# Performance work log

Measured on AMD Instinct MI355X. Metric: run time of the kernel, lower is better.

The kernel has to match this reference:

```python
import jax, jax.numpy as jnp
import numpy as np

N = 50000
K = 4
D_IN = 256
D_OUT = 64
E = 800000

def setup_inputs() -> dict:
    key = jax.random.key(0)
    k1, k2, k3, k4, k5 = jax.random.split(key, 5)
    x = jax.random.normal(k1, (N, K, D_IN), dtype=jnp.float32)
    weight = jax.random.normal(k2, (D_IN, D_OUT), dtype=jnp.float32) * (1.0 / np.sqrt(D_IN))
    adj_rows = jax.random.randint(k3, (E,), 0, N, dtype=jnp.int32)
    adj_cols = jax.random.randint(k4, (E,), 0, N, dtype=jnp.int32)
    adj_vals = jax.random.uniform(k5, (E,), dtype=jnp.float32)
    return {"x": x, "weight": weight, "adj_rows": adj_rows, "adj_cols": adj_cols, "adj_vals": adj_vals}

def reference(x, weight, adj_rows, adj_cols, adj_vals):
    # x: [N, K, D_in]; weight: [D_in, D_out]
    # dropout p=0.0 / eval mode -> identity
    # support = x @ W for every sample k, vectorized over K
    support = jnp.einsum('nkd,df->nkf', x, weight)          # [N, K, D_out]
    # sparse adj matmul: out[r] += vals[e] * support[cols[e]]
    msgs = adj_vals[:, None, None] * support[adj_cols]       # [E, K, D_out]
    out = jax.ops.segment_sum(msgs, adj_rows, num_segments=N)  # [N, K, D_out]
    return jax.nn.relu(out)
```

## Files before the change

kernel.cpp:

```cpp
#include <hip/hip_runtime.h>
#include <stdint.h>

#define D_IN   256
#define D_OUT  64
#define KHEADS 4
#define ROWLEN 256
#define GBM    128
#define LDW    264
#define CAP    128

typedef __attribute__((ext_vector_type(8))) short bf16x8;
typedef __attribute__((ext_vector_type(4))) float f32x4;

__device__ __forceinline__ unsigned cvt_pk_bf16(float lo, float hi) {
  unsigned r;
  asm("v_cvt_pk_bf16_f32 %0, %1, %2" : "=v"(r) : "v"(lo), "v"(hi));
  return r;
}

__device__ __forceinline__ bf16x8 pack8(float4 a, float4 b) {
  union { unsigned u[4]; bf16x8 v; } r;
  r.u[0] = cvt_pk_bf16(a.x, a.y);
  r.u[1] = cvt_pk_bf16(a.z, a.w);
  r.u[2] = cvt_pk_bf16(b.x, b.y);
  r.u[3] = cvt_pk_bf16(b.z, b.w);
  return r.v;
}

__device__ __forceinline__ void gemm_body(const float* __restrict__ X,
                                          const float* __restrict__ W,
                                          signed char* __restrict__ Sq,
                                          float* __restrict__ scaleArr,
                                          int M, int Nnodes, int gb) {
  __shared__ unsigned short lWt[64 * LDW];
  const int t    = threadIdx.x;
  const int wave = t >> 6;
  const int lane = t & 63;
  const int q    = lane >> 4;
  const int l16  = lane & 15;
  const long row0 = (long)gb * GBM;

#pragma unroll
  for (int j = 0; j < 16; ++j) {
    int flat = t + j * 256;
    int kr   = flat >> 4;
    int nn   = (flat & 15) << 2;
    float4 v = *(const float4*)&W[(size_t)kr * D_OUT + nn];
    unsigned p0 = cvt_pk_bf16(v.x, v.y);
    unsigned p1 = cvt_pk_bf16(v.z, v.w);
    lWt[(nn + 0) * LDW + kr] = (unsigned short)(p0 & 0xffffu);
    lWt[(nn + 1) * LDW + kr] = (unsigned short)(p0 >> 16);
    lWt[(nn + 2) * LDW + kr] = (unsigned short)(p1 & 0xffffu);
    lWt[(nn + 3) * LDW + kr] = (unsigned short)(p1 >> 16);
  }
  __syncthreads();

  long r0 = row0 + wave * 32 + l16;       if (r0 > (long)M - 1) r0 = M - 1;
  long r1 = row0 + wave * 32 + 16 + l16;  if (r1 > (long)M - 1) r1 = M - 1;
  const float* __restrict__ x0 = X + r0 * D_IN + q * 8;
  const float* __restrict__ x1 = X + r1 * D_IN + q * 8;

  f32x4 acc[2][4];
#pragma unroll
  for (int rb = 0; rb < 2; ++rb)
#pragma unroll
    for (int cb = 0; cb < 4; ++cb) acc[rb][cb] = (f32x4){0.f, 0.f, 0.f, 0.f};

  float4 c00 = *(const float4*)(x0);
  float4 c01 = *(const float4*)(x0 + 4);
  float4 c10 = *(const float4*)(x1);
  float4 c11 = *(const float4*)(x1 + 4);
#pragma unroll
  for (int s = 0; s < 8; ++s) {
    float4 n00, n01, n10, n11;
    if (s < 7) {
      const float* p0 = x0 + (s + 1) * 32;
      const float* p1 = x1 + (s + 1) * 32;
      n00 = *(const float4*)(p0); n01 = *(const float4*)(p0 + 4);
      n10 = *(const float4*)(p1); n11 = *(const float4*)(p1 + 4);
    }
    bf16x8 a0 = pack8(c00, c01);
    bf16x8 a1 = pack8(c10, c11);
    const unsigned short* wb = &lWt[l16 * LDW + s * 32 + q * 8];
#pragma unroll
    for (int cb = 0; cb < 4; ++cb) {
      bf16x8 b = *(const bf16x8*)(wb + cb * 16 * LDW);
      acc[0][cb] = __builtin_amdgcn_mfma_f32_16x16x32_bf16(a0, b, acc[0][cb], 0, 0, 0);
      acc[1][cb] = __builtin_amdgcn_mfma_f32_16x16x32_bf16(a1, b, acc[1][cb], 0, 0, 0);
    }
    if (s < 7) { c00 = n00; c01 = n01; c10 = n10; c11 = n11; }
  }

  float nm0 = 0.f, nm1 = 0.f;
#pragma unroll
  for (int cb = 0; cb < 4; ++cb)
#pragma unroll
    for (int reg = 0; reg < 4; ++reg) {
      nm0 = fmaxf(nm0, fabsf(acc[0][cb][reg]));
      nm1 = fmaxf(nm1, fabsf(acc[1][cb][reg]));
    }
#pragma unroll
  for (int d = 1; d < 16; d <<= 1) {
    nm0 = fmaxf(nm0, __shfl_xor(nm0, d, 64));
    nm1 = fmaxf(nm1, __shfl_xor(nm1, d, 64));
  }
  const float inv0 = (nm0 > 0.f) ? 127.f / nm0 : 0.f;
  const float inv1 = (nm1 > 0.f) ? 127.f / nm1 : 0.f;
  const int node_base = gb * 32 + wave * 8;
  if (l16 == 0) {
    int n0 = node_base + q;
    int n1 = node_base + 4 + q;
    if (n0 < Nnodes) scaleArr[n0] = nm0 / 127.f;
    if (n1 < Nnodes) scaleArr[n1] = nm1 / 127.f;
  }
#pragma unroll
  for (int rb = 0; rb < 2; ++rb) {
    const float inv = rb ? inv1 : inv0;
#pragma unroll
    for (int cb = 0; cb < 4; ++cb)
#pragma unroll
      for (int reg = 0; reg < 4; ++reg) {
        long r = row0 + wave * 32 + rb * 16 + q * 4 + reg;
        if (r < M) {
          int qi = (int)rintf(acc[rb][cb][reg] * inv);
          Sq[r * D_OUT + cb * 16 + l16] = (signed char)qi;
        }
      }
  }
}

__device__ __forceinline__ void place_body(const int* __restrict__ rows,
                                           const int* __restrict__ cols,
                                           const float* __restrict__ vals,
                                           int* __restrict__ cnt,
                                           uint2* __restrict__ ecv, int E, int pb) {
  int e = pb * 256 + threadIdx.x;
  if (e < E) {
    int r = rows[e];
    int c = cols[e];
    float v = vals[e];
    int pos = atomicAdd(&cnt[r], 1);
    if (pos < CAP)
      ecv[((size_t)r << 7) + pos] = make_uint2((unsigned)c, __float_as_uint(v));
  }
}

__global__ __launch_bounds__(256) void fused_phase1(
    const float* __restrict__ X, const float* __restrict__ W,
    signed char* __restrict__ Sq, float* __restrict__ scaleArr,
    const int* __restrict__ rows, const int* __restrict__ cols,
    const float* __restrict__ vals, int* __restrict__ cnt,
    uint2* __restrict__ ecv, int M, int Nnodes, int E, int G, int P) {
  const int bid = blockIdx.x;
  const int g = bid / 3, r3 = bid - 3 * g;
  if (r3 == 0) {
    if (g < G) gemm_body(X, W, Sq, scaleArr, M, Nnodes, g);
  } else {
    int pb = 2 * g + r3 - 1;
    if (pb < P) place_body(rows, cols, vals, cnt, ecv, E, pb);
  }
}

__global__ __launch_bounds__(256) void gather_kernel(const int* __restrict__ Sqi,
                                                     const float* __restrict__ scaleArr,
                                                     const int* __restrict__ cnt,
                                                     const uint2* __restrict__ ecv,
                                                     float* __restrict__ out, int n) {
  const int lane = threadIdx.x & 63;
  const int r = blockIdx.x * 4 + (threadIdx.x >> 6);
  if (r >= n) return;
  int deg = cnt[r];
  if (deg > CAP) deg = CAP;
  const uint2* __restrict__ bucket = ecv + ((size_t)r << 7);

  uint2 b0 = bucket[lane];
  unsigned mc = (lane < deg) ? b0.x : 0u;
  float    mv = (lane < deg) ? __uint_as_float(b0.y) * scaleArr[mc] : 0.f;

  float4 a0 = make_float4(0.f, 0.f, 0.f, 0.f);
  float4 a1 = a0, a2 = a0, a3 = a0;
  const int d0 = deg < 64 ? deg : 64;
  for (int i = 0; i < d0; i += 4) {
    const int e1 = (i + 1 < d0) ? i + 1 : d0 - 1;
    const int e2 = (i + 2 < d0) ? i + 2 : d0 - 1;
    const int e3 = (i + 3 < d0) ? i + 3 : d0 - 1;
    unsigned c0 = __shfl(mc, i);
    unsigned c1 = __shfl(mc, e1);
    unsigned c2 = __shfl(mc, e2);
    unsigned c3 = __shfl(mc, e3);
    float v0 = __shfl(mv, i);
    float v1 = (i + 1 < d0) ? __shfl(mv, e1) : 0.f;
    float v2 = (i + 2 < d0) ? __shfl(mv, e2) : 0.f;
    float v3 = (i + 3 < d0) ? __shfl(mv, e3) : 0.f;
    int w0 = Sqi[(size_t)c0 * 64 + lane];
    int w1 = Sqi[(size_t)c1 * 64 + lane];
    int w2 = Sqi[(size_t)c2 * 64 + lane];
    int w3 = Sqi[(size_t)c3 * 64 + lane];
    a0.x += v0 * (float)(w0 << 24 >> 24); a0.y += v0 * (float)(w0 << 16 >> 24);
    a0.z += v0 * (float)(w0 <<  8 >> 24); a0.w += v0 * (float)(w0 >> 24);
    a1.x += v1 * (float)(w1 << 24 >> 24); a1.y += v1 * (float)(w1 << 16 >> 24);
    a1.z += v1 * (float)(w1 <<  8 >> 24); a1.w += v1 * (float)(w1 >> 24);
    a2.x += v2 * (float)(w2 << 24 >> 24); a2.y += v2 * (float)(w2 << 16 >> 24);
    a2.z += v2 * (float)(w2 <<  8 >> 24); a2.w += v2 * (float)(w2 >> 24);
    a3.x += v3 * (float)(w3 << 24 >> 24); a3.y += v3 * (float)(w3 << 16 >> 24);
    a3.z += v3 * (float)(w3 <<  8 >> 24); a3.w += v3 * (float)(w3 >> 24);
  }
  if (deg > 64) {
    uint2 b1 = bucket[64 + lane];
    unsigned mc1 = (64 + lane < deg) ? b1.x : 0u;
    float    mv1 = (64 + lane < deg) ? __uint_as_float(b1.y) * scaleArr[mc1] : 0.f;
    for (int e = 64; e < deg; ++e) {
      unsigned c = __shfl(mc1, e - 64);
      float    v = __shfl(mv1, e - 64);
      int w = Sqi[(size_t)c * 64 + lane];
      a0.x += v * (float)(w << 24 >> 24); a0.y += v * (float)(w << 16 >> 24);
      a0.z += v * (float)(w <<  8 >> 24); a0.w += v * (float)(w >> 24);
    }
  }
  f32x4 res;
  res[0] = fmaxf(a0.x + a1.x + a2.x + a3.x, 0.f);
  res[1] = fmaxf(a0.y + a1.y + a2.y + a3.y, 0.f);
  res[2] = fmaxf(a0.z + a1.z + a2.z + a3.z, 0.f);
  res[3] = fmaxf(a0.w + a1.w + a2.w + a3.w, 0.f);
  __builtin_nontemporal_store(res, (f32x4*)&out[(size_t)r * ROWLEN + (lane << 2)]);
}

extern "C" void kernel_launch(void* const* d_in, const int* in_sizes, int n_in,
                              void* d_out, int out_size, void* d_ws, size_t ws_size,
                              hipStream_t stream) {
  const float* x    = (const float*)d_in[0];
  const float* w    = (const float*)d_in[1];
  const int*   rows = (const int*)d_in[2];
  const int*   cols = (const int*)d_in[3];
  const float* vals = (const float*)d_in[4];
  float* out = (float*)d_out;

  const int E = in_sizes[2];
  const int N = in_sizes[0] / (KHEADS * D_IN);
  const int M = N * KHEADS;

  char* ws = (char*)d_ws;
  size_t o = 0;
  signed char* Sq = (signed char*)(ws + o); o += (size_t)M * D_OUT;
  o = (o + 15) & ~(size_t)15;
  float* scaleArr = (float*)(ws + o); o += (size_t)N * sizeof(float);
  o = (o + 15) & ~(size_t)15;
  int* cnt = (int*)(ws + o); o += (size_t)N * sizeof(int);
  o = (o + 15) & ~(size_t)15;
  uint2* ecv = (uint2*)(ws + o);

  hipMemsetAsync(cnt, 0, (size_t)N * sizeof(int), stream);

  const int G = (M + GBM - 1) / GBM;
  const int P = (E + 255) / 256;
  fused_phase1<<<3 * G, 256, 0, stream>>>(x, w, Sq, scaleArr, rows, cols, vals,
                                          cnt, ecv, M, N, E, G, P);
  gather_kernel<<<(N + 3) / 4, 256, 0, stream>>>((const int*)Sq, scaleArr, cnt, ecv, out, N);
}
```

Before: 366.2 us.

## Precompute transposed bf16 weight once; widen gather unroll to eight edges

A small prep kernel converts W to bf16 and writes it already transposed with the padded LDS layout. Each GEMM block can then fill shared memory with plain 16-byte copies instead of converting and doing scattered 2-byte transposed LDS stores. The gather loop now issues eight independent int8 row loads per iteration instead of four, to expose more memory-level parallelism. The bucket is read with a nontemporal load. This adds one extra kernel launch and a little more register pressure in the gather.

After: 365.1 us. Within noise of the previous version (-0.3%).

```diff
diff --git a/kernel.cpp b/kernel.cpp
--- a/kernel.cpp
+++ b/kernel.cpp
@@ -7,6 +7,7 @@
 #define ROWLEN 256
 #define GBM    128
 #define LDW    264
+#define WBT_B  (64 * LDW * 2)
 #define CAP    128
 
 typedef __attribute__((ext_vector_type(8))) short bf16x8;
@@ -27,12 +28,26 @@
   return r.v;
 }
 
+__global__ __launch_bounds__(256) void prep_w(const float* __restrict__ W,
+                                              unsigned short* __restrict__ WbT) {
+  int idx = blockIdx.x * 256 + threadIdx.x;
+  int n  = idx >> 6;
+  int k0 = (idx & 63) << 2;
+  float w0 = W[(size_t)(k0 + 0) * D_OUT + n];
+  float w1 = W[(size_t)(k0 + 1) * D_OUT + n];
+  float w2 = W[(size_t)(k0 + 2) * D_OUT + n];
+  float w3 = W[(size_t)(k0 + 3) * D_OUT + n];
+  unsigned p0 = cvt_pk_bf16(w0, w1);
+  unsigned p1 = cvt_pk_bf16(w2, w3);
+  *(uint2*)&WbT[(size_t)n * LDW + k0] = make_uint2(p0, p1);
+}
+
 __device__ __forceinline__ void gemm_body(const float* __restrict__ X,
-                                          const float* __restrict__ W,
+                                          const unsigned short* __restrict__ WbT,
                                           signed char* __restrict__ Sq,
                                           float* __restrict__ scaleArr,
                                           int M, int Nnodes, int gb) {
-  __shared__ unsigned short lWt[64 * LDW];
+  __shared__ __align__(16) unsigned short lWt[64 * LDW];
   const int t    = threadIdx.x;
   const int wave = t >> 6;
   const int lane = t & 63;
@@ -40,18 +55,14 @@
   const int l16  = lane & 15;
   const long row0 = (long)gb * GBM;
 
-#pragma unroll
-  for (int j = 0; j < 16; ++j) {
-    int flat = t + j * 256;
-    int kr   = flat >> 4;
-    int nn   = (flat & 15) << 2;
-    float4 v = *(const float4*)&W[(size_t)kr * D_OUT + nn];
-    unsigned p0 = cvt_pk_bf16(v.x, v.y);
-    unsigned p1 = cvt_pk_bf16(v.z, v.w);
-    lWt[(nn + 0) * LDW + kr] = (unsigned short)(p0 & 0xffffu);
-    lWt[(nn + 1) * LDW + kr] = (unsigned short)(p0 >> 16);
-    lWt[(nn + 2) * LDW + kr] = (unsigned short)(p1 & 0xffffu);
-    lWt[(nn + 3) * LDW + kr] = (unsigned short)(p1 >> 16);
+  {
+    const uint4* __restrict__ src = (const uint4*)WbT;
+    uint4* dst = (uint4*)lWt;
+#pragma unroll
+    for (int r2 = 0; r2 < 9; ++r2) {
+      int slot = t + r2 * 256;
+      if (slot < WBT_B / 16) dst[slot] = src[slot];
+    }
   }
   __syncthreads();
 
@@ -146,7 +157,7 @@
 }
 
 __global__ __launch_bounds__(256) void fused_phase1(
-    const float* __restrict__ X, const float* __restrict__ W,
+    const float* __restrict__ X, const unsigned short* __restrict__ WbT,
     signed char* __restrict__ Sq, float* __restrict__ scaleArr,
     const int* __restrict__ rows, const int* __restrict__ cols,
     const float* __restrict__ vals, int* __restrict__ cnt,
@@ -154,7 +165,7 @@
   const int bid = blockIdx.x;
   const int g = bid / 3, r3 = bid - 3 * g;
   if (r3 == 0) {
-    if (g < G) gemm_body(X, W, Sq, scaleArr, M, Nnodes, g);
+    if (g < G) gemm_body(X, WbT, Sq, scaleArr, M, Nnodes, g);
   } else {
     int pb = 2 * g + r3 - 1;
     if (pb < P) place_body(rows, cols, vals, cnt, ecv, E, pb);
@@ -173,37 +184,36 @@
   if (deg > CAP) deg = CAP;
   const uint2* __restrict__ bucket = ecv + ((size_t)r << 7);
 
-  uint2 b0 = bucket[lane];
-  unsigned mc = (lane < deg) ? b0.x : 0u;
-  float    mv = (lane < deg) ? __uint_as_float(b0.y) * scaleArr[mc] : 0.f;
+  unsigned long long bl =
+      __builtin_nontemporal_load((const unsigned long long*)bucket + lane);
+  unsigned mc = (lane < deg) ? (unsigned)bl : 0u;
+  float    mv = (lane < deg) ? __uint_as_float((unsigned)(bl >> 32)) * scaleArr[mc] : 0.f;
 
   float4 a0 = make_float4(0.f, 0.f, 0.f, 0.f);
   float4 a1 = a0, a2 = a0, a3 = a0;
   const int d0 = deg < 64 ? deg : 64;
-  for (int i = 0; i < d0; i += 4) {
-    const int e1 = (i + 1 < d0) ? i + 1 : d0 - 1;
-    const int e2 = (i + 2 < d0) ? i + 2 : d0 - 1;
-    const int e3 = (i + 3 < d0) ? i + 3 : d0 - 1;
-    unsigned c0 = __shfl(mc, i);
-    unsigned c1 = __shfl(mc, e1);
-    unsigned c2 = __shfl(mc, e2);
-    unsigned c3 = __shfl(mc, e3);
-    float v0 = __shfl(mv, i);
-    float v1 = (i + 1 < d0) ? __shfl(mv, e1) : 0.f;
-    float v2 = (i + 2 < d0) ? __shfl(mv, e2) : 0.f;
-    float v3 = (i + 3 < d0) ? __shfl(mv, e3) : 0.f;
-    int w0 = Sqi[(size_t)c0 * 64 + lane];
-    int w1 = Sqi[(size_t)c1 * 64 + lane];
-    int w2 = Sqi[(size_t)c2 * 64 + lane];
-    int w3 = Sqi[(size_t)c3 * 64 + lane];
-    a0.x += v0 * (float)(w0 << 24 >> 24); a0.y += v0 * (float)(w0 << 16 >> 24);
-    a0.z += v0 * (float)(w0 <<  8 >> 24); a0.w += v0 * (float)(w0 >> 24);
-    a1.x += v1 * (float)(w1 << 24 >> 24); a1.y += v1 * (float)(w1 << 16 >> 24);
-    a1.z += v1 * (float)(w1 <<  8 >> 24); a1.w += v1 * (float)(w1 >> 24);
-    a2.x += v2 * (float)(w2 << 24 >> 24); a2.y += v2 * (float)(w2 << 16 >> 24);
-    a2.z += v2 * (float)(w2 <<  8 >> 24); a2.w += v2 * (float)(w2 >> 24);
-    a3.x += v3 * (float)(w3 << 24 >> 24); a3.y += v3 * (float)(w3 << 16 >> 24);
-    a3.z += v3 * (float)(w3 <<  8 >> 24); a3.w += v3 * (float)(w3 >> 24);
+  for (int i = 0; i < d0; i += 8) {
+    unsigned cc[8]; float vv[8]; int ww[8];
+#pragma unroll
+    for (int u = 0; u < 8; ++u) {
+      int e = i + u;
+      int ec = e < d0 ? e : d0 - 1;
+      cc[u] = __shfl(mc, ec);
+      float vraw = __shfl(mv, ec);
+      vv[u] = (e < d0) ? vraw : 0.f;
+    }
+#pragma unroll
+    for (int u = 0; u < 8; ++u) ww[u] = Sqi[(size_t)cc[u] * 64 + lane];
+#pragma unroll
+    for (int u = 0; u < 8; ++u) {
+      float4& a = ((u & 3) == 0) ? a0 : (((u & 3) == 1) ? a1 : (((u & 3) == 2) ? a2 : a3));
+      const float v = vv[u];
+      const int   w = ww[u];
+      a.x += v * (float)(w << 24 >> 24);
+      a.y += v * (float)(w << 16 >> 24);
+      a.z += v * (float)(w <<  8 >> 24);
+      a.w += v * (float)(w >> 24);
+    }
   }
   if (deg > 64) {
     uint2 b1 = bucket[64 + lane];
@@ -246,6 +256,8 @@
   float* scaleArr = (float*)(ws + o); o += (size_t)N * sizeof(float);
   o = (o + 15) & ~(size_t)15;
   int* cnt = (int*)(ws + o); o += (size_t)N * sizeof(int);
+  o = (o + 63) & ~(size_t)63;
+  unsigned short* WbT = (unsigned short*)(ws + o); o += WBT_B;
   o = (o + 15) & ~(size_t)15;
   uint2* ecv = (uint2*)(ws + o);
 
@@ -253,7 +265,8 @@
 
   const int G = (M + GBM - 1) / GBM;
   const int P = (E + 255) / 256;
-  fused_phase1<<<3 * G, 256, 0, stream>>>(x, w, Sq, scaleArr, rows, cols, vals,
+  prep_w<<<16, 256, 0, stream>>>(w, WbT);
+  fused_phase1<<<3 * G, 256, 0, stream>>>(x, WbT, Sq, scaleArr, rows, cols, vals,
                                           cnt, ecv, M, N, E, G, P);
   gather_kernel<<<(N + 3) / 4, 256, 0, stream>>>((const int*)Sq, scaleArr, cnt, ecv, out, N);
 }
```
